# Kernel optimization log

Hardware: AMD Instinct MI355X
Metric: run time of the kernel (lower is better)

Reference implementation:

```python
import jax, jax.numpy as jnp
import numpy as np

N_NODES = 60000
N_EDGES = 120000
N_GRAPHS = 2048
ATOM_DIM = 4
H = 192            # hidden_dim
NL = 5             # n_layers
ND = 200           # n_descriptors
EDGE_DIM = 1


def setup_inputs() -> dict:
    key = jax.random.key(0)
    ks = jax.random.split(key, 16)

    def w(k, shape, fan_in):
        return jax.random.normal(k, shape, jnp.float32) * (1.0 / np.sqrt(fan_in))

    M_IN = 2 * H + EDGE_DIM  # message MLP input: [x_src, x_dst, edge_attr]
    M_H = 2 * H              # MPNNLayer(hidden_dim=hidden_dim*2)
    inp = {
        "atom_features": jax.random.normal(ks[0], (N_NODES, ATOM_DIM), jnp.float32),
        "edge_attr": jax.random.normal(ks[1], (N_EDGES, EDGE_DIM), jnp.float32),
        "edge_index": jax.random.randint(ks[2], (2, N_EDGES), 0, N_NODES),
        "batch": jnp.sort(jax.random.randint(ks[3], (N_NODES,), 0, N_GRAPHS)),
        # atom encoder: Linear + GELU + LayerNorm
        "enc_w": w(ks[4], (ATOM_DIM, H), ATOM_DIM), "enc_b": jnp.zeros((H,), jnp.float32),
        "enc_ln_g": jnp.ones((H,), jnp.float32), "enc_ln_b": jnp.zeros((H,), jnp.float32),
        # 5 MPNN layers (stacked params)
        "msg_w1": w(ks[5], (NL, M_IN, M_H), M_IN), "msg_b1": jnp.zeros((NL, M_H), jnp.float32),
        "msg_w2": w(ks[6], (NL, M_H, H), M_H), "msg_b2": jnp.zeros((NL, H), jnp.float32),
        "upd_w": w(ks[7], (NL, 2 * H, H), 2 * H), "upd_b": jnp.zeros((NL, H), jnp.float32),
        "ln_g": jnp.ones((NL, H), jnp.float32), "ln_b": jnp.zeros((NL, H), jnp.float32),
        # head MLP: 2H -> H -> H//2 -> ND
        "h1_w": w(ks[8], (2 * H, H), 2 * H), "h1_b": jnp.zeros((H,), jnp.float32),
        "h2_w": w(ks[9], (H, H // 2), H), "h2_b": jnp.zeros((H // 2,), jnp.float32),
        "h3_w": w(ks[10], (H // 2, ND), H // 2), "h3_b": jnp.zeros((ND,), jnp.float32),
    }
    return inp


def _ln(x, g, b, eps=1e-5):
    mu = x.mean(-1, keepdims=True)
    v = x.var(-1, keepdims=True)
    return (x - mu) / jnp.sqrt(v + eps) * g + b


def _gelu(x):
    return jax.nn.gelu(x, approximate=False)  # torch nn.GELU (erf)


def _forward(atom_features, edge_attr, enc_w, enc_b, enc_ln_g, enc_ln_b,
             msg_w1, msg_b1, msg_w2, msg_b2, upd_w, upd_b, ln_g, ln_b,
             h1_w, h1_b, h2_w, h2_b, h3_w, h3_b, edge_index, batch):
    src, dst = edge_index[0], edge_index[1]
    x = _ln(_gelu(atom_features @ enc_w + enc_b), enc_ln_g, enc_ln_b)  # [N, H]
    for l in range(NL):
        # gather endpoints -> message MLP -> scatter-sum to dst
        m_in = jnp.concatenate([x[src], x[dst], edge_attr], axis=-1)   # [E, 2H+1]
        m = _gelu(m_in @ msg_w1[l] + msg_b1[l]) @ msg_w2[l] + msg_b2[l]  # [E, H]
        agg = jax.ops.segment_sum(m, dst, num_segments=N_NODES)        # [N, H]
        x_new = _gelu(jnp.concatenate([x, agg], axis=-1) @ upd_w[l] + upd_b[l])
        x = _ln(x + x_new, ln_g[l], ln_b[l])  # residual + LN (dropout = eval identity)
    # per-graph mean/max pooling (segment reductions)
    cnt = jax.ops.segment_sum(jnp.ones((x.shape[0],), x.dtype), batch, num_segments=N_GRAPHS)
    s = jax.ops.segment_sum(x, batch, num_segments=N_GRAPHS)
    mean_pool = jnp.where(cnt[:, None] > 0, s / jnp.maximum(cnt, 1.0)[:, None], 0.0)
    max_pool = jax.ops.segment_max(x, batch, num_segments=N_GRAPHS)  # -inf for empty, as torch
    g = jnp.concatenate([mean_pool, max_pool], axis=-1)  # [G, 2H]
    h = _gelu(g @ h1_w + h1_b)
    h = _gelu(h @ h2_w + h2_b)
    return h @ h3_w + h3_b  # [G, ND]


def reference(atom_features, edge_attr, edge_index, batch, enc_w, enc_b, enc_ln_g, enc_ln_b,
              msg_w1, msg_b1, msg_w2, msg_b2, upd_w, upd_b, ln_g, ln_b,
              h1_w, h1_b, h2_w, h2_b, h3_w, h3_b):
    return _forward(atom_features, edge_attr, enc_w, enc_b, enc_ln_g, enc_ln_b,
                    msg_w1, msg_b1, msg_w2, msg_b2, upd_w, upd_b, ln_g, ln_b,
                    h1_w, h1_b, h2_w, h2_b, h3_w, h3_b, edge_index, batch)
```

## Files before the change

### kernel.cpp

```cpp
#include <hip/hip_runtime.h>

#define H 192
#define NL 5
#define NN 60000
#define NE 120000
#define NG 2048
#define ND 200
#define LDA 392
#define NT 128
#define LDU 200

typedef __bf16 bfrag __attribute__((ext_vector_type(8)));
typedef __bf16 bf16x4 __attribute__((ext_vector_type(4)));
typedef float f32x4 __attribute__((ext_vector_type(4)));

__device__ __forceinline__ unsigned short f2bf(float f) {
  union { float f; unsigned u; } v; v.f = f;
  return (unsigned short)((v.u + 0x7FFFu + ((v.u >> 16) & 1u)) >> 16);
}
__device__ __forceinline__ float bflo(unsigned u) {
  union { unsigned u; float f; } v; v.u = u << 16; return v.f;
}
__device__ __forceinline__ float bfhi(unsigned u) {
  union { unsigned u; float f; } v; v.u = u & 0xffff0000u; return v.f;
}
__device__ __forceinline__ float gelu(float x) {
  const float t = exp2f(x * (-2.3020922f - 0.10293942f * x * x));
  return x * __builtin_amdgcn_rcpf(1.f + t);
}

__global__ __launch_bounds__(256) void fold_kernel(
    const float* __restrict__ msg_w2, const float* __restrict__ upd_w,
    const float* __restrict__ msg_b2, float* __restrict__ W2p,
    float* __restrict__ v2) {
  __shared__ float row4[4][192];
  const int bid = blockIdx.x;
  const int l = bid / 97, sub = bid % 97;
  const int j = threadIdx.x;
  if (j < 192) {
    if (sub < 96) {
      const int k0 = sub * 4;
#pragma unroll
      for (int rr = 0; rr < 4; ++rr)
        row4[rr][j] = msg_w2[(size_t)l * 384 * 192 + (size_t)(k0 + rr) * 192 + j];
    } else {
      row4[0][j] = msg_b2[l * 192 + j];
    }
  }
  __syncthreads();
  if (j >= 192) return;
  const float* Ua = upd_w + (size_t)l * 384 * 192 + (size_t)192 * 192;
  float acc[4] = {0.f, 0.f, 0.f, 0.f};
  for (int t = 0; t < 192; ++t) {
    const float u = Ua[t * 192 + j];
#pragma unroll
    for (int rr = 0; rr < 4; ++rr) acc[rr] += row4[rr][t] * u;
  }
  if (sub < 96) {
    const int k0 = sub * 4;
#pragma unroll
    for (int rr = 0; rr < 4; ++rr)
      W2p[(size_t)l * 384 * 192 + (size_t)(k0 + rr) * 192 + j] = acc[rr];
  } else {
    v2[l * 192 + j] = acc[0];
  }
}

__global__ __launch_bounds__(256) void prep_kernel(
    const float* __restrict__ msg_w1, const float* __restrict__ W2p,
    const float* __restrict__ upd_w, const float* __restrict__ h1_w,
    const float* __restrict__ h2_w, const float* __restrict__ h3_w,
    unsigned short* __restrict__ W1f, float* __restrict__ w1last,
    unsigned short* __restrict__ W2f, unsigned short* __restrict__ Uxf,
    unsigned short* __restrict__ h1f, unsigned short* __restrict__ h2f,
    unsigned short* __restrict__ h3f) {
  int idx = blockIdx.x * 256 + threadIdx.x;
  const int SW1 = NL * 147456;
  const int S2 = NL * 384;
  const int SW2 = NL * 73728;
  const int SUX = NL * 36864;
  if (idx < SW1) {
    int l = idx / 147456, r = idx % 147456;
    int i = r & 7, lane = (r >> 3) & 63, t = r >> 9;
    int kk = t % 12, jblk = t / 12;
    int j = jblk * 16 + (lane & 15);
    int k = kk * 32 + ((lane >> 4) << 3) + i;
    W1f[idx] = f2bf(msg_w1[(size_t)l * 385 * 384 + (size_t)k * 384 + j]);
    return;
  }
  idx -= SW1;
  if (idx < S2) {
    int l = idx / 384, j = idx % 384;
    w1last[idx] = msg_w1[(size_t)l * 385 * 384 + 384 * 384 + j];
    return;
  }
  idx -= S2;
  if (idx < SW2) {
    int l = idx / 73728, r = idx % 73728;
    int i = r & 7, lane = (r >> 3) & 63, t = r >> 9;
    int kk = t % 12, jblk = t / 12;
    int j = jblk * 16 + (lane & 15);
    int k = kk * 32 + ((lane >> 4) << 3) + i;
    W2f[idx] = f2bf(W2p[(size_t)l * 384 * 192 + (size_t)k * 192 + j]);
    return;
  }
  idx -= SW2;
  if (idx < SUX) {
    int l = idx / 36864, r = idx % 36864;
    int i = r & 7, lane = (r >> 3) & 63, t = r >> 9;
    int kk = t % 6, jblk = t / 6;
    int j = jblk * 16 + (lane & 15);
    int k = kk * 32 + ((lane >> 4) << 3) + i;
    Uxf[idx] = f2bf(upd_w[(size_t)l * 384 * 192 + (size_t)k * 192 + j]);
    return;
  }
  idx -= SUX;
  if (idx < 73728) {
    int i = idx & 7, lane = (idx >> 3) & 63, t = idx >> 9;
    int kk = t % 12, jblk = t / 12;
    int j = jblk * 16 + (lane & 15);
    int k = kk * 32 + ((lane >> 4) << 3) + i;
    h1f[idx] = f2bf(h1_w[(size_t)k * 192 + j]);
    return;
  }
  idx -= 73728;
  if (idx < 18432) {
    int i = idx & 7, lane = (idx >> 3) & 63, t = idx >> 9;
    int kk = t % 6, jblk = t / 6;
    int j = jblk * 16 + (lane & 15);
    int k = kk * 32 + ((lane >> 4) << 3) + i;
    h2f[idx] = f2bf(h2_w[(size_t)k * 96 + j]);
    return;
  }
  idx -= 18432;
  if (idx < 19968) {
    int i = idx & 7, lane = (idx >> 3) & 63, t = idx >> 9;
    int kk = t % 3, jblk = t / 3;
    int j = jblk * 16 + (lane & 15);
    int k = kk * 32 + ((lane >> 4) << 3) + i;
    h3f[idx] = (j < 200) ? f2bf(h3_w[(size_t)k * 200 + j]) : (unsigned short)0;
    return;
  }
}

__global__ __launch_bounds__(256) void enc_kernel(
    const float* __restrict__ af, const float* __restrict__ w,
    const float* __restrict__ b, const float* __restrict__ g,
    const float* __restrict__ bb, __bf16* __restrict__ xb) {
  const int node = blockIdx.x * 4 + (threadIdx.x >> 6);
  const int lane = threadIdx.x & 63;
  if (node >= NN) return;
  const float a0 = af[node * 4 + 0], a1 = af[node * 4 + 1];
  const float a2 = af[node * 4 + 2], a3 = af[node * 4 + 3];
  float v[3], s = 0.f, ss = 0.f;
#pragma unroll
  for (int i = 0; i < 3; ++i) {
    const int j = lane + i * 64;
    float o = a0 * w[j] + a1 * w[H + j] + a2 * w[2 * H + j] + a3 * w[3 * H + j] + b[j];
    o = gelu(o);
    v[i] = o; s += o; ss += o * o;
  }
#pragma unroll
  for (int m = 1; m < 64; m <<= 1) { s += __shfl_xor(s, m); ss += __shfl_xor(ss, m); }
  const float mu = s * (1.f / H);
  float var = ss * (1.f / H) - mu * mu;
  const float rstd = rsqrtf(fmaxf(var, 0.f) + 1e-5f);
#pragma unroll
  for (int i = 0; i < 3; ++i) {
    const int j = lane + i * 64;
    xb[(size_t)node * H + j] = (__bf16)((v[i] - mu) * rstd * g[j] + bb[j]);
  }
}

__global__ __launch_bounds__(256) void csr_count(const int* __restrict__ ei,
                                                 int* __restrict__ deg) {
  const int e = blockIdx.x * 256 + threadIdx.x;
  if (e < NE) atomicAdd(&deg[ei[NE + e]], 1);
}

__global__ __launch_bounds__(1024) void csr_scan(const int* __restrict__ deg,
                                                 int* __restrict__ start) {
  __shared__ int wsum[16];
  const int tid = threadIdx.x, lane = tid & 63, wv = tid >> 6;
  int carry = 0;
  for (int base = 0; base < NN; base += 1024) {
    const int i = base + tid;
    int v = (i < NN) ? deg[i] : 0;
    int s = v;
#pragma unroll
    for (int d = 1; d < 64; d <<= 1) {
      int t = __shfl_up(s, d);
      if (lane >= d) s += t;
    }
    if (lane == 63) wsum[wv] = s;
    __syncthreads();
    if (wv == 0) {
      int ws_ = (lane < 16) ? wsum[lane] : 0;
#pragma unroll
      for (int d = 1; d < 16; d <<= 1) {
        int t = __shfl_up(ws_, d);
        if (lane >= d) ws_ += t;
      }
      if (lane < 16) wsum[lane] = ws_;
    }
    __syncthreads();
    const int woff = (wv == 0) ? 0 : wsum[wv - 1];
    if (i < NN) start[i] = carry + woff + s - v;
    carry += wsum[15];
    __syncthreads();
  }
  if (tid == 0) start[NN] = NE;
}

__global__ __launch_bounds__(256) void csr_fill(const int* __restrict__ ei,
                                                const int* __restrict__ start,
                                                int* __restrict__ cur,
                                                int* __restrict__ pos) {
  const int e = blockIdx.x * 256 + threadIdx.x;
  if (e < NE) {
    const int d = ei[NE + e];
    const int p = start[d] + atomicAdd(&cur[d], 1);
    pos[e] = p;
  }
}

__global__ __launch_bounds__(256) void gseg_kernel(const int* __restrict__ batch,
                                                   int* __restrict__ gstart,
                                                   int* __restrict__ gend) {
  const int i = blockIdx.x * 256 + threadIdx.x;
  if (i >= NN) return;
  const int b = batch[i];
  if (i == 0 || batch[i - 1] != b) gstart[b] = i;
  if (i == NN - 1 || batch[i + 1] != b) gend[b] = i + 1;
}

__global__ __launch_bounds__(512, 4) void msg_kernel(
    const __bf16* __restrict__ xb, const int* __restrict__ ei,
    const float* __restrict__ ea, const int* __restrict__ pos,
    const unsigned short* __restrict__ W1f, const float* __restrict__ w1last,
    const float* __restrict__ b1, const unsigned short* __restrict__ W2f,
    unsigned short* __restrict__ m) {
  __shared__ unsigned short A[64 * LDA];
  __shared__ float eaS[64];
  __shared__ int posS[64];
  const int tid = threadIdx.x;
  const int wave = tid >> 6, lane = tid & 63;
  const int lrow = lane & 15, kgrp = lane >> 4;
  const int tile = blockIdx.x * 64;

  if (tid < 64) {
    eaS[tid] = ea[tile + tid];
    posS[tid] = pos[tile + tid];
  }
  {
    const int r = tid >> 3, s = tid & 7;
    const int e = tile + r;
    const uint4* ps = (const uint4*)(xb + (size_t)ei[e] * H);
    const uint4* pd = (const uint4*)(xb + (size_t)ei[NE + e] * H);
#pragma unroll
    for (int i = 0; i < 3; ++i)
      *(uint4*)(&A[r * LDA + (s + 8 * i) * 8]) = ps[s + 8 * i];
#pragma unroll
    for (int i = 3; i < 6; ++i)
      *(uint4*)(&A[r * LDA + (s + 8 * i) * 8]) = pd[s + 8 * i - 24];
  }
  __syncthreads();

  const int jb16 = wave * 3;
  f32x4 acc[3][4];
#pragma unroll
  for (int mf = 0; mf < 3; ++mf)
#pragma unroll
    for (int eb = 0; eb < 4; ++eb)
#pragma unroll
      for (int q = 0; q < 4; ++q) acc[mf][eb][q] = 0.f;

#pragma unroll 2
  for (int kk = 0; kk < 12; ++kk) {
    const int k0 = kk * 32 + kgrp * 8;
    bfrag bF[4];
#pragma unroll
    for (int eb = 0; eb < 4; ++eb)
      bF[eb] = *(const bfrag*)(&A[(eb * 16 + lrow) * LDA + k0]);
#pragma unroll
    for (int mf = 0; mf < 3; ++mf) {
      const bfrag aF = *(const bfrag*)(W1f + ((size_t)((jb16 + mf) * 12 + kk) * 64 + lane) * 8);
#pragma unroll
      for (int eb = 0; eb < 4; ++eb)
        acc[mf][eb] = __builtin_amdgcn_mfma_f32_16x16x32_bf16(aF, bF[eb], acc[mf][eb], 0, 0, 0);
    }
  }
  __syncthreads();

#pragma unroll
  for (int mf = 0; mf < 3; ++mf) {
    const int j0 = (jb16 + mf) * 16 + kgrp * 4;
    const float bi0 = b1[j0], bi1 = b1[j0 + 1], bi2 = b1[j0 + 2], bi3 = b1[j0 + 3];
    const float wl0 = w1last[j0], wl1 = w1last[j0 + 1], wl2 = w1last[j0 + 2], wl3 = w1last[j0 + 3];
#pragma unroll
    for (int eb = 0; eb < 4; ++eb) {
      const int e = eb * 16 + lrow;
      const float eav = eaS[e];
      bf16x4 v;
      v[0] = (__bf16)gelu(acc[mf][eb][0] + bi0 + eav * wl0);
      v[1] = (__bf16)gelu(acc[mf][eb][1] + bi1 + eav * wl1);
      v[2] = (__bf16)gelu(acc[mf][eb][2] + bi2 + eav * wl2);
      v[3] = (__bf16)gelu(acc[mf][eb][3] + bi3 + eav * wl3);
      *(bf16x4*)(&A[e * LDA + j0]) = v;
    }
  }
  __syncthreads();

  const int jcnt2 = (wave < 4) ? 2 : 1;
  const int j2b0 = (wave < 4) ? (wave * 2) : (4 + wave);
  f32x4 acc2[2][4];
#pragma unroll
  for (int a = 0; a < 2; ++a)
#pragma unroll
    for (int eb = 0; eb < 4; ++eb)
#pragma unroll
      for (int q = 0; q < 4; ++q) acc2[a][eb][q] = 0.f;

#pragma unroll 2
  for (int kk = 0; kk < 12; ++kk) {
    const int k0 = kk * 32 + kgrp * 8;
    bfrag bF[4];
#pragma unroll
    for (int eb = 0; eb < 4; ++eb)
      bF[eb] = *(const bfrag*)(&A[(eb * 16 + lrow) * LDA + k0]);
#pragma unroll
    for (int a = 0; a < 2; ++a) {
      if (a < jcnt2) {
        const bfrag aF = *(const bfrag*)(W2f + ((size_t)((j2b0 + a) * 12 + kk) * 64 + lane) * 8);
#pragma unroll
        for (int eb = 0; eb < 4; ++eb)
          acc2[a][eb] = __builtin_amdgcn_mfma_f32_16x16x32_bf16(aF, bF[eb], acc2[a][eb], 0, 0, 0);
      }
    }
  }
#pragma unroll
  for (int a = 0; a < 2; ++a) {
    if (a < jcnt2) {
      const int j0 = (j2b0 + a) * 16 + kgrp * 4;
#pragma unroll
      for (int eb = 0; eb < 4; ++eb) {
        const int e = eb * 16 + lrow;
        bf16x4 v;
        v[0] = (__bf16)acc2[a][eb][0];
        v[1] = (__bf16)acc2[a][eb][1];
        v[2] = (__bf16)acc2[a][eb][2];
        v[3] = (__bf16)acc2[a][eb][3];
        *(bf16x4*)(m + (size_t)posS[e] * H + j0) = v;
      }
    }
  }
}

__global__ __launch_bounds__(512, 4) void upd_kernel(
    const unsigned short* __restrict__ Uxf, const float* __restrict__ ub,
    const float* __restrict__ v2, const float* __restrict__ lng,
    const float* __restrict__ lnb, const unsigned short* __restrict__ m,
    const int* __restrict__ start, __bf16* xb) {
  __shared__ unsigned short A[NT * LDU];
  __shared__ float wsm[8][NT];
  __shared__ float wsq[8][NT];
  __shared__ float mur[NT], rsr[NT];
  __shared__ float degS[NT];
  const int tid = threadIdx.x;
  const int wave = tid >> 6, lane = tid & 63;
  const int lrow = lane & 15, kgrp = lane >> 4;
  const int tile = blockIdx.x * NT;

  const int r = tid >> 2, q4 = tid & 3;
  const int node = tile + r;
  if (node < NN) {
    const uint4* px = (const uint4*)(xb + (size_t)node * H + q4 * 48);
#pragma unroll
    for (int i = 0; i < 6; ++i)
      *(uint4*)(&A[r * LDU + q4 * 48 + i * 8]) = px[i];
  } else {
#pragma unroll
    for (int i = 0; i < 6; ++i)
      *(uint4*)(&A[r * LDU + q4 * 48 + i * 8]) = make_uint4(0, 0, 0, 0);
  }
  __syncthreads();

  const int jcnt = (wave < 4) ? 2 : 1;
  const int jb0 = (wave < 4) ? (wave * 2) : (4 + wave);

  f32x4 acc[2][8];
#pragma unroll
  for (int a = 0; a < 2; ++a)
#pragma unroll
    for (int eb = 0; eb < 8; ++eb)
#pragma unroll
      for (int q = 0; q < 4; ++q) acc[a][eb][q] = 0.f;

#pragma unroll 1
  for (int kk = 0; kk < 6; ++kk) {
    const int k0 = kk * 32 + kgrp * 8;
    bfrag bF[8];
#pragma unroll
    for (int eb = 0; eb < 8; ++eb)
      bF[eb] = *(const bfrag*)(&A[(eb * 16 + lrow) * LDU + k0]);
#pragma unroll
    for (int a = 0; a < 2; ++a) {
      if (a < jcnt) {
        const bfrag aF = *(const bfrag*)(Uxf + ((size_t)((jb0 + a) * 6 + kk) * 64 + lane) * 8);
#pragma unroll
        for (int eb = 0; eb < 8; ++eb)
          acc[a][eb] = __builtin_amdgcn_mfma_f32_16x16x32_bf16(aF, bF[eb], acc[a][eb], 0, 0, 0);
      }
    }
  }
  __syncthreads();

  if (node < NN) {
    const int p0 = start[node], p1 = start[node + 1];
    if (q4 == 0) degS[r] = (float)(p1 - p0);
#pragma unroll
    for (int hh = 0; hh < 2; ++hh) {
      const int c0 = q4 * 48 + hh * 24;
      float av[24];
#pragma unroll
      for (int i = 0; i < 24; ++i) av[i] = 0.f;
      for (int p = p0; p < p1; ++p) {
        const uint4* mr = (const uint4*)(m + (size_t)p * H + c0);
#pragma unroll
        for (int i = 0; i < 3; ++i) {
          const uint4 u = mr[i];
          av[i * 8 + 0] += bflo(u.x); av[i * 8 + 1] += bfhi(u.x);
          av[i * 8 + 2] += bflo(u.y); av[i * 8 + 3] += bfhi(u.y);
          av[i * 8 + 4] += bflo(u.z); av[i * 8 + 5] += bfhi(u.z);
          av[i * 8 + 6] += bflo(u.w); av[i * 8 + 7] += bfhi(u.w);
        }
      }
#pragma unroll
      for (int i = 0; i < 24; i += 4) {
        bf16x4 v;
        v[0] = (__bf16)av[i]; v[1] = (__bf16)av[i + 1];
        v[2] = (__bf16)av[i + 2]; v[3] = (__bf16)av[i + 3];
        *(bf16x4*)(&A[r * LDU + c0 + i]) = v;
      }
    }
  } else {
    if (q4 == 0) degS[r] = 0.f;
#pragma unroll
    for (int i = 0; i < 48; i += 8)
      *(uint4*)(&A[r * LDU + q4 * 48 + i]) = make_uint4(0, 0, 0, 0);
  }
  __syncthreads();

  float lsum[8], lsq[8];
#pragma unroll
  for (int eb = 0; eb < 8; ++eb) { lsum[eb] = 0.f; lsq[eb] = 0.f; }
#pragma unroll
  for (int a = 0; a < 2; ++a) {
    if (a < jcnt) {
      const int jb = (jb0 + a) * 16 + kgrp * 4;
      const float4 ub4 = *(const float4*)(ub + jb);
      const float4 v24 = *(const float4*)(v2 + jb);
#pragma unroll
      for (int eb = 0; eb < 8; ++eb) {
        const int nc = eb * 16 + lrow;
        const int n2 = tile + nc;
        if (n2 < NN) {
          const bf16x4 ag = *(const bf16x4*)(&A[nc * LDU + jb]);
          const float d = degS[nc];
          const bf16x4 xr = *(const bf16x4*)(xb + (size_t)n2 * H + jb);
          acc[a][eb][0] = (float)xr[0] + gelu(acc[a][eb][0] + (float)ag[0] + d * v24.x + ub4.x);
          acc[a][eb][1] = (float)xr[1] + gelu(acc[a][eb][1] + (float)ag[1] + d * v24.y + ub4.y);
          acc[a][eb][2] = (float)xr[2] + gelu(acc[a][eb][2] + (float)ag[2] + d * v24.z + ub4.z);
          acc[a][eb][3] = (float)xr[3] + gelu(acc[a][eb][3] + (float)ag[3] + d * v24.w + ub4.w);
        } else {
          acc[a][eb][0] = 0.f; acc[a][eb][1] = 0.f;
          acc[a][eb][2] = 0.f; acc[a][eb][3] = 0.f;
        }
#pragma unroll
        for (int q = 0; q < 4; ++q) {
          lsum[eb] += acc[a][eb][q];
          lsq[eb] += acc[a][eb][q] * acc[a][eb][q];
        }
      }
    }
  }
#pragma unroll
  for (int eb = 0; eb < 8; ++eb) {
    lsum[eb] += __shfl_xor(lsum[eb], 16);
    lsum[eb] += __shfl_xor(lsum[eb], 32);
    lsq[eb] += __shfl_xor(lsq[eb], 16);
    lsq[eb] += __shfl_xor(lsq[eb], 32);
  }
  if (kgrp == 0) {
#pragma unroll
    for (int eb = 0; eb < 8; ++eb) {
      wsm[wave][eb * 16 + lrow] = lsum[eb];
      wsq[wave][eb * 16 + lrow] = lsq[eb];
    }
  }
  __syncthreads();
  if (tid < NT) {
    float s = 0.f, sq = 0.f;
#pragma unroll
    for (int w2 = 0; w2 < 8; ++w2) { s += wsm[w2][tid]; sq += wsq[w2][tid]; }
    const float mu = s * (1.f / H);
    float var = sq * (1.f / H) - mu * mu;
    mur[tid] = mu;
    rsr[tid] = rsqrtf(fmaxf(var, 0.f) + 1e-5f);
  }
  __syncthreads();
#pragma unroll
  for (int a = 0; a < 2; ++a) {
    if (a < jcnt) {
      const int jb = (jb0 + a) * 16 + kgrp * 4;
      const float4 g4 = *(const float4*)(lng + jb);
      const float4 b4 = *(const float4*)(lnb + jb);
#pragma unroll
      for (int eb = 0; eb < 8; ++eb) {
        const int nc = eb * 16 + lrow;
        const int n2 = tile + nc;
        if (n2 < NN) {
          const float mu = mur[nc], rs = rsr[nc];
          bf16x4 ob;
          ob[0] = (__bf16)((acc[a][eb][0] - mu) * rs * g4.x + b4.x);
          ob[1] = (__bf16)((acc[a][eb][1] - mu) * rs * g4.y + b4.y);
          ob[2] = (__bf16)((acc[a][eb][2] - mu) * rs * g4.z + b4.z);
          ob[3] = (__bf16)((acc[a][eb][3] - mu) * rs * g4.w + b4.w);
          *(bf16x4*)(xb + (size_t)n2 * H + jb) = ob;
        }
      }
    }
  }
}

__global__ __launch_bounds__(256) void pool_kernel(
    const __bf16* __restrict__ xb, const int* __restrict__ gstart,
    const int* __restrict__ gend, __bf16* __restrict__ Gb) {
  const int w = threadIdx.x >> 6, lane = threadIdx.x & 63;
  const int gi = blockIdx.x * 4 + w;
  const int n0 = gstart[gi], n1 = gend[gi];
  float sm[3] = {0.f, 0.f, 0.f};
  float mx[3] = {-INFINITY, -INFINITY, -INFINITY};
  for (int n = n0; n < n1; ++n) {
#pragma unroll
    for (int i = 0; i < 3; ++i) {
      const float v = (float)xb[(size_t)n * H + lane + i * 64];
      sm[i] += v; mx[i] = fmaxf(mx[i], v);
    }
  }
  const int cnt = n1 - n0;
  const float inv = cnt > 0 ? 1.f / (float)cnt : 0.f;
#pragma unroll
  for (int i = 0; i < 3; ++i) {
    const int j = lane + i * 64;
    Gb[(size_t)gi * 384 + j] = (__bf16)(sm[i] * inv);
    Gb[(size_t)gi * 384 + 192 + j] = (__bf16)mx[i];
  }
}

__global__ __launch_bounds__(512) void head_kernel(
    const __bf16* __restrict__ Gb,
    const unsigned short* __restrict__ h1f, const float* __restrict__ h1b,
    const unsigned short* __restrict__ h2f, const float* __restrict__ h2b,
    const unsigned short* __restrict__ h3f, const float* __restrict__ h3b,
    float* __restrict__ out) {
  __shared__ unsigned short A[32 * LDA];
  const int tid = threadIdx.x;
  const int wave = tid >> 6, lane = tid & 63;
  const int lrow = lane & 15, kgrp = lane >> 4;
  const int tile = blockIdx.x * 32;

  {
    const int r = tid >> 4, s = tid & 15;
    const uint4* pg = (const uint4*)(Gb + (size_t)(tile + r) * 384);
#pragma unroll
    for (int i = 0; i < 3; ++i)
      *(uint4*)(&A[r * LDA + (s + 16 * i) * 8]) = pg[s + 16 * i];
  }
  __syncthreads();

  const int jcnt1 = (wave < 4) ? 2 : 1;
  const int jb1 = (wave < 4) ? (wave * 2) : (4 + wave);
  f32x4 acc[2][2];
#pragma unroll
  for (int a = 0; a < 2; ++a)
#pragma unroll
    for (int eb = 0; eb < 2; ++eb)
#pragma unroll
      for (int q = 0; q < 4; ++q) acc[a][eb][q] = 0.f;
#pragma unroll 2
  for (int kk = 0; kk < 12; ++kk) {
    const int k0 = kk * 32 + kgrp * 8;
    bfrag bF[2];
#pragma unroll
    for (int eb = 0; eb < 2; ++eb)
      bF[eb] = *(const bfrag*)(&A[(eb * 16 + lrow) * LDA + k0]);
#pragma unroll
    for (int a = 0; a < 2; ++a) {
      if (a < jcnt1) {
        const bfrag aF = *(const bfrag*)(h1f + ((size_t)((jb1 + a) * 12 + kk) * 64 + lane) * 8);
#pragma unroll
        for (int eb = 0; eb < 2; ++eb)
          acc[a][eb] = __builtin_amdgcn_mfma_f32_16x16x32_bf16(aF, bF[eb], acc[a][eb], 0, 0, 0);
      }
    }
  }
  __syncthreads();
#pragma unroll
  for (int a = 0; a < 2; ++a) {
    if (a < jcnt1) {
      const int j0 = (jb1 + a) * 16 + kgrp * 4;
      const float4 b4 = *(const float4*)(h1b + j0);
#pragma unroll
      for (int eb = 0; eb < 2; ++eb) {
        const int g = eb * 16 + lrow;
        bf16x4 v;
        v[0] = (__bf16)gelu(acc[a][eb][0] + b4.x);
        v[1] = (__bf16)gelu(acc[a][eb][1] + b4.y);
        v[2] = (__bf16)gelu(acc[a][eb][2] + b4.z);
        v[3] = (__bf16)gelu(acc[a][eb][3] + b4.w);
        *(bf16x4*)(&A[g * LDA + j0]) = v;
      }
    }
  }
  __syncthreads();

  f32x4 acc2[2];
#pragma unroll
  for (int eb = 0; eb < 2; ++eb)
#pragma unroll
    for (int q = 0; q < 4; ++q) acc2[eb][q] = 0.f;
  if (wave < 6) {
#pragma unroll 2
    for (int kk = 0; kk < 6; ++kk) {
      const int k0 = kk * 32 + kgrp * 8;
      bfrag bF[2];
#pragma unroll
      for (int eb = 0; eb < 2; ++eb)
        bF[eb] = *(const bfrag*)(&A[(eb * 16 + lrow) * LDA + k0]);
      const bfrag aF = *(const bfrag*)(h2f + ((size_t)(wave * 6 + kk) * 64 + lane) * 8);
#pragma unroll
      for (int eb = 0; eb < 2; ++eb)
        acc2[eb] = __builtin_amdgcn_mfma_f32_16x16x32_bf16(aF, bF[eb], acc2[eb], 0, 0, 0);
    }
  }
  __syncthreads();
  if (wave < 6) {
    const int j0 = wave * 16 + kgrp * 4;
    const float4 b4 = *(const float4*)(h2b + j0);
#pragma unroll
    for (int eb = 0; eb < 2; ++eb) {
      const int g = eb * 16 + lrow;
      bf16x4 v;
      v[0] = (__bf16)gelu(acc2[eb][0] + b4.x);
      v[1] = (__bf16)gelu(acc2[eb][1] + b4.y);
      v[2] = (__bf16)gelu(acc2[eb][2] + b4.z);
      v[3] = (__bf16)gelu(acc2[eb][3] + b4.w);
      *(bf16x4*)(&A[g * LDA + 192 + j0]) = v;
    }
  }
  __syncthreads();

  const int jcnt3 = (wave < 5) ? 2 : 1;
  const int jb3 = (wave < 5) ? (wave * 2) : (wave + 5);
  f32x4 acc3[2][2];
#pragma unroll
  for (int a = 0; a < 2; ++a)
#pragma unroll
    for (int eb = 0; eb < 2; ++eb)
#pragma unroll
      for (int q = 0; q < 4; ++q) acc3[a][eb][q] = 0.f;
#pragma unroll
  for (int kk = 0; kk < 3; ++kk) {
    const int k0 = 192 + kk * 32 + kgrp * 8;
    bfrag bF[2];
#pragma unroll
    for (int eb = 0; eb < 2; ++eb)
      bF[eb] = *(const bfrag*)(&A[(eb * 16 + lrow) * LDA + k0]);
#pragma unroll
    for (int a = 0; a < 2; ++a) {
      if (a < jcnt3) {
        const bfrag aF = *(const bfrag*)(h3f + ((size_t)((jb3 + a) * 3 + kk) * 64 + lane) * 8);
#pragma unroll
        for (int eb = 0; eb < 2; ++eb)
          acc3[a][eb] = __builtin_amdgcn_mfma_f32_16x16x32_bf16(aF, bF[eb], acc3[a][eb], 0, 0, 0);
      }
    }
  }
#pragma unroll
  for (int a = 0; a < 2; ++a) {
    if (a < jcnt3) {
      const int jb = jb3 + a;
      const int j0 = jb * 16 + kgrp * 4;
#pragma unroll
      for (int eb = 0; eb < 2; ++eb) {
        const int g = tile + eb * 16 + lrow;
        if (jb < 12) {
          const float4 b4 = *(const float4*)(h3b + j0);
          float4 o;
          o.x = acc3[a][eb][0] + b4.x;
          o.y = acc3[a][eb][1] + b4.y;
          o.z = acc3[a][eb][2] + b4.z;
          o.w = acc3[a][eb][3] + b4.w;
          *(float4*)(out + (size_t)g * ND + j0) = o;
        } else {
#pragma unroll
          for (int t = 0; t < 4; ++t) {
            const int j = j0 + t;
            if (j < ND) out[(size_t)g * ND + j] = acc3[a][eb][t] + h3b[j];
          }
        }
      }
    }
  }
}

extern "C" void kernel_launch(void* const* d_in, const int* in_sizes, int n_in,
                              void* d_out, int out_size, void* d_ws, size_t ws_size,
                              hipStream_t stream) {
  const float* atom   = (const float*)d_in[0];
  const float* ea     = (const float*)d_in[1];
  const int*   ei     = (const int*)d_in[2];
  const int*   batch  = (const int*)d_in[3];
  const float* enc_w  = (const float*)d_in[4];
  const float* enc_b  = (const float*)d_in[5];
  const float* enc_lng= (const float*)d_in[6];
  const float* enc_lnb= (const float*)d_in[7];
  const float* msg_w1 = (const float*)d_in[8];
  const float* msg_b1 = (const float*)d_in[9];
  const float* msg_w2 = (const float*)d_in[10];
  const float* msg_b2 = (const float*)d_in[11];
  const float* upd_w  = (const float*)d_in[12];
  const float* upd_b  = (const float*)d_in[13];
  const float* ln_g   = (const float*)d_in[14];
  const float* ln_b   = (const float*)d_in[15];
  const float* h1_w   = (const float*)d_in[16];
  const float* h1_b   = (const float*)d_in[17];
  const float* h2_w   = (const float*)d_in[18];
  const float* h2_b   = (const float*)d_in[19];
  const float* h3_w   = (const float*)d_in[20];
  const float* h3_b   = (const float*)d_in[21];
  float* out = (float*)d_out;

  char* ws = (char*)d_ws;
  size_t off = 0;
  auto alloc = [&](size_t bytes) -> void* {
    void* p = ws + off;
    off = (off + bytes + 255) & ~(size_t)255;
    return p;
  };
  __bf16* xb          = (__bf16*)alloc((size_t)NN * H * 2);
  unsigned short* msg = (unsigned short*)alloc((size_t)NE * H * 2);
  unsigned short* W1f = (unsigned short*)alloc((size_t)NL * 147456 * 2);
  float* w1last       = (float*)alloc((size_t)NL * 384 * 4);
  unsigned short* W2f = (unsigned short*)alloc((size_t)NL * 73728 * 2);
  unsigned short* Uxf = (unsigned short*)alloc((size_t)NL * 36864 * 2);
  float* W2p          = (float*)alloc((size_t)NL * 384 * 192 * 4);
  float* v2           = (float*)alloc((size_t)NL * 192 * 4);
  unsigned short* h1f = (unsigned short*)alloc((size_t)73728 * 2);
  unsigned short* h2f = (unsigned short*)alloc((size_t)18432 * 2);
  unsigned short* h3f = (unsigned short*)alloc((size_t)19968 * 2);
  __bf16* Gb          = (__bf16*)alloc((size_t)NG * 384 * 2);
  int* deg            = (int*)alloc((size_t)NN * 4);
  int* cstart         = (int*)alloc((size_t)(NN + 1) * 4);
  int* pos            = (int*)alloc((size_t)NE * 4);
  int* gstart         = (int*)alloc((size_t)NG * 4);
  int* gend           = (int*)alloc((size_t)NG * 4);

  fold_kernel<<<NL * 97, 256, 0, stream>>>(msg_w2, upd_w, msg_b2, W2p, v2);
  prep_kernel<<<5486, 256, 0, stream>>>(msg_w1, W2p, upd_w, h1_w, h2_w, h3_w,
                                        W1f, w1last, W2f, Uxf, h1f, h2f, h3f);
  enc_kernel<<<NN / 4, 256, 0, stream>>>(atom, enc_w, enc_b, enc_lng, enc_lnb, xb);

  hipMemsetAsync(deg, 0, (size_t)NN * 4, stream);
  csr_count<<<(NE + 255) / 256, 256, 0, stream>>>(ei, deg);
  csr_scan<<<1, 1024, 0, stream>>>(deg, cstart);
  hipMemsetAsync(deg, 0, (size_t)NN * 4, stream);
  csr_fill<<<(NE + 255) / 256, 256, 0, stream>>>(ei, cstart, deg, pos);

  hipMemsetAsync(gstart, 0, (size_t)NG * 4, stream);
  hipMemsetAsync(gend, 0, (size_t)NG * 4, stream);
  gseg_kernel<<<(NN + 255) / 256, 256, 0, stream>>>(batch, gstart, gend);

  for (int l = 0; l < NL; ++l) {
    msg_kernel<<<NE / 64, 512, 0, stream>>>(
        xb, ei, ea, pos, W1f + (size_t)l * 147456, w1last + l * 384,
        msg_b1 + l * 384, W2f + (size_t)l * 73728, msg);
    upd_kernel<<<(NN + NT - 1) / NT, 512, 0, stream>>>(
        Uxf + (size_t)l * 36864, upd_b + l * 192, v2 + l * 192,
        ln_g + l * 192, ln_b + l * 192, msg, cstart, xb);
  }
  pool_kernel<<<NG / 4, 256, 0, stream>>>(xb, gstart, gend, Gb);
  head_kernel<<<NG / 32, 512, 0, stream>>>(Gb, h1f, h1_b, h2f, h2_b, h3f, h3_b, out);
}
```

Before: 756.5 us.

## Make msg_kernel persistent and prefetch next tile's gathered rows into registers

The message kernel now launches a fixed grid of 512 blocks that loop over 64-edge tiles, instead of one block per tile. While the MLP for the current tile runs, each thread loads the next tile's source and destination node rows, edge attributes and positions into registers, then writes them to shared memory once the tile is finished. The goal is to hide the latency of the random gathers behind the MFMA work. In exchange it raises register pressure with six uint4 values per thread, and 512 blocks may leave some CUs underused at launch_bounds(512,4).

```diff
diff --git a/kernel.cpp b/kernel.cpp
--- a/kernel.cpp
+++ b/kernel.cpp
@@ -9,6 +9,7 @@
 #define LDA 392
 #define NT 128
 #define LDU 200
+#define MSGB 512
 
 typedef __bf16 bfrag __attribute__((ext_vector_type(8)));
 typedef __bf16 bf16x4 __attribute__((ext_vector_type(4)));
@@ -246,112 +247,139 @@
   const int tid = threadIdx.x;
   const int wave = tid >> 6, lane = tid & 63;
   const int lrow = lane & 15, kgrp = lane >> 4;
-  const int tile = blockIdx.x * 64;
-
-  if (tid < 64) {
-    eaS[tid] = ea[tile + tid];
-    posS[tid] = pos[tile + tid];
-  }
+  const int sr = tid >> 3, sc = tid & 7;
+  const int NTILES = NE / 64;
+
   {
-    const int r = tid >> 3, s = tid & 7;
-    const int e = tile + r;
+    const int tile = blockIdx.x * 64;
+    if (tid < 64) { eaS[tid] = ea[tile + tid]; posS[tid] = pos[tile + tid]; }
+    const int e = tile + sr;
     const uint4* ps = (const uint4*)(xb + (size_t)ei[e] * H);
     const uint4* pd = (const uint4*)(xb + (size_t)ei[NE + e] * H);
 #pragma unroll
     for (int i = 0; i < 3; ++i)
-      *(uint4*)(&A[r * LDA + (s + 8 * i) * 8]) = ps[s + 8 * i];
+      *(uint4*)(&A[sr * LDA + (sc + 8 * i) * 8]) = ps[sc + 8 * i];
 #pragma unroll
     for (int i = 3; i < 6; ++i)
-      *(uint4*)(&A[r * LDA + (s + 8 * i) * 8]) = pd[s + 8 * i - 24];
-  }
-  __syncthreads();
-
-  const int jb16 = wave * 3;
-  f32x4 acc[3][4];
-#pragma unroll
-  for (int mf = 0; mf < 3; ++mf)
-#pragma unroll
-    for (int eb = 0; eb < 4; ++eb)
-#pragma unroll
-      for (int q = 0; q < 4; ++q) acc[mf][eb][q] = 0.f;
+      *(uint4*)(&A[sr * LDA + (sc + 8 * i) * 8]) = pd[sc + 8 * i - 24];
+  }
+  __syncthreads();
+
+  for (int tile_idx = blockIdx.x; tile_idx < NTILES; tile_idx += MSGB) {
+    const int tile = tile_idx * 64;
+    const bool has_next = (tile_idx + MSGB) < NTILES;
+
+    uint4 pf[6];
+    float eaN = 0.f;
+    int posN = 0;
+    if (has_next) {
+      const int t2 = (tile_idx + MSGB) * 64;
+      const int e2 = t2 + sr;
+      const uint4* ps = (const uint4*)(xb + (size_t)ei[e2] * H);
+      const uint4* pd = (const uint4*)(xb + (size_t)ei[NE + e2] * H);
+#pragma unroll
+      for (int i = 0; i < 3; ++i) pf[i] = ps[sc + 8 * i];
+#pragma unroll
+      for (int i = 3; i < 6; ++i) pf[i] = pd[sc + 8 * i - 24];
+      if (tid < 64) { eaN = ea[t2 + tid]; posN = pos[t2 + tid]; }
+    }
+
+    const int jb16 = wave * 3;
+    f32x4 acc[3][4];
+#pragma unroll
+    for (int mf = 0; mf < 3; ++mf)
+#pragma unroll
+      for (int eb = 0; eb < 4; ++eb)
+#pragma unroll
+        for (int q = 0; q < 4; ++q) acc[mf][eb][q] = 0.f;
 
 #pragma unroll 2
-  for (int kk = 0; kk < 12; ++kk) {
-    const int k0 = kk * 32 + kgrp * 8;
-    bfrag bF[4];
-#pragma unroll
-    for (int eb = 0; eb < 4; ++eb)
-      bF[eb] = *(const bfrag*)(&A[(eb * 16 + lrow) * LDA + k0]);
+    for (int kk = 0; kk < 12; ++kk) {
+      const int k0 = kk * 32 + kgrp * 8;
+      bfrag bF[4];
+#pragma unroll
+      for (int eb = 0; eb < 4; ++eb)
+        bF[eb] = *(const bfrag*)(&A[(eb * 16 + lrow) * LDA + k0]);
+#pragma unroll
+      for (int mf = 0; mf < 3; ++mf) {
+        const bfrag aF = *(const bfrag*)(W1f + ((size_t)((jb16 + mf) * 12 + kk) * 64 + lane) * 8);
+#pragma unroll
+        for (int eb = 0; eb < 4; ++eb)
+          acc[mf][eb] = __builtin_amdgcn_mfma_f32_16x16x32_bf16(aF, bF[eb], acc[mf][eb], 0, 0, 0);
+      }
+    }
+    __syncthreads();
+
 #pragma unroll
     for (int mf = 0; mf < 3; ++mf) {
-      const bfrag aF = *(const bfrag*)(W1f + ((size_t)((jb16 + mf) * 12 + kk) * 64 + lane) * 8);
+      const int j0 = (jb16 + mf) * 16 + kgrp * 4;
+      const float bi0 = b1[j0], bi1 = b1[j0 + 1], bi2 = b1[j0 + 2], bi3 = b1[j0 + 3];
+      const float wl0 = w1last[j0], wl1 = w1last[j0 + 1], wl2 = w1last[j0 + 2], wl3 = w1last[j0 + 3];
+#pragma unroll
+      for (int eb = 0; eb < 4; ++eb) {
+        const int e = eb * 16 + lrow;
+        const float eav = eaS[e];
+        bf16x4 v;
+        v[0] = (__bf16)gelu(acc[mf][eb][0] + bi0 + eav * wl0);
+        v[1] = (__bf16)gelu(acc[mf][eb][1] + bi1 + eav * wl1);
+        v[2] = (__bf16)gelu(acc[mf][eb][2] + bi2 + eav * wl2);
+        v[3] = (__bf16)gelu(acc[mf][eb][3] + bi3 + eav * wl3);
+        *(bf16x4*)(&A[e * LDA + j0]) = v;
+      }
+    }
+    __syncthreads();
+
+    const int jcnt2 = (wave < 4) ? 2 : 1;
+    const int j2b0 = (wave < 4) ? (wave * 2) : (4 + wave);
+    f32x4 acc2[2][4];
+#pragma unroll
+    for (int a = 0; a < 2; ++a)
 #pragma unroll
       for (int eb = 0; eb < 4; ++eb)
-        acc[mf][eb] = __builtin_amdgcn_mfma_f32_16x16x32_bf16(aF, bF[eb], acc[mf][eb], 0, 0, 0);
-    }
-  }
-  __syncthreads();
-
-#pragma unroll
-  for (int mf = 0; mf < 3; ++mf) {
-    const int j0 = (jb16 + mf) * 16 + kgrp * 4;
-    const float bi0 = b1[j0], bi1 = b1[j0 + 1], bi2 = b1[j0 + 2], bi3 = b1[j0 + 3];
-    const float wl0 = w1last[j0], wl1 = w1last[j0 + 1], wl2 = w1last[j0 + 2], wl3 = w1last[j0 + 3];
-#pragma unroll
-    for (int eb = 0; eb < 4; ++eb) {
-      const int e = eb * 16 + lrow;
-      const float eav = eaS[e];
-      bf16x4 v;
-      v[0] = (__bf16)gelu(acc[mf][eb][0] + bi0 + eav * wl0);
-      v[1] = (__bf16)gelu(acc[mf][eb][1] + bi1 + eav * wl1);
-      v[2] = (__bf16)gelu(acc[mf][eb][2] + bi2 + eav * wl2);
-      v[3] = (__bf16)gelu(acc[mf][eb][3] + bi3 + eav * wl3);
-      *(bf16x4*)(&A[e * LDA + j0]) = v;
-    }
-  }
-  __syncthreads();
-
-  const int jcnt2 = (wave < 4) ? 2 : 1;
-  const int j2b0 = (wave < 4) ? (wave * 2) : (4 + wave);
-  f32x4 acc2[2][4];
-#pragma unroll
-  for (int a = 0; a < 2; ++a)
-#pragma unroll
-    for (int eb = 0; eb < 4; ++eb)
-#pragma unroll
-      for (int q = 0; q < 4; ++q) acc2[a][eb][q] = 0.f;
+#pragma unroll
+        for (int q = 0; q < 4; ++q) acc2[a][eb][q] = 0.f;
 
 #pragma unroll 2
-  for (int kk = 0; kk < 12; ++kk) {
-    const int k0 = kk * 32 + kgrp * 8;
-    bfrag bF[4];
-#pragma unroll
-    for (int eb = 0; eb < 4; ++eb)
-      bF[eb] = *(const bfrag*)(&A[(eb * 16 + lrow) * LDA + k0]);
+    for (int kk = 0; kk < 12; ++kk) {
+      const int k0 = kk * 32 + kgrp * 8;
+      bfrag bF[4];
+#pragma unroll
+      for (int eb = 0; eb < 4; ++eb)
+        bF[eb] = *(const bfrag*)(&A[(eb * 16 + lrow) * LDA + k0]);
+#pragma unroll
+      for (int a = 0; a < 2; ++a) {
+        if (a < jcnt2) {
+          const bfrag aF = *(const bfrag*)(W2f + ((size_t)((j2b0 + a) * 12 + kk) * 64 + lane) * 8);
+#pragma unroll
+          for (int eb = 0; eb < 4; ++eb)
+            acc2[a][eb] = __builtin_amdgcn_mfma_f32_16x16x32_bf16(aF, bF[eb], acc2[a][eb], 0, 0, 0);
+        }
+      }
+    }
 #pragma unroll
     for (int a = 0; a < 2; ++a) {
       if (a < jcnt2) {
-        const bfrag aF = *(const bfrag*)(W2f + ((size_t)((j2b0 + a) * 12 + kk) * 64 + lane) * 8);
-#pragma unroll
-        for (int eb = 0; eb < 4; ++eb)
-          acc2[a][eb] = __builtin_amdgcn_mfma_f32_16x16x32_bf16(aF, bF[eb], acc2[a][eb], 0, 0, 0);
-      }
-    }
-  }
-#pragma unroll
-  for (int a = 0; a < 2; ++a) {
-    if (a < jcnt2) {
-      const int j0 = (j2b0 + a) * 16 + kgrp * 4;
-#pragma unroll
-      for (int eb = 0; eb < 4; ++eb) {
-        const int e = eb * 16 + lrow;
-        bf16x4 v;
-        v[0] = (__bf16)acc2[a][eb][0];
-        v[1] = (__bf16)acc2[a][eb][1];
-        v[2] = (__bf16)acc2[a][eb][2];
-        v[3] = (__bf16)acc2[a][eb][3];
-        *(bf16x4*)(m + (size_t)posS[e] * H + j0) = v;
-      }
+        const int j0 = (j2b0 + a) * 16 + kgrp * 4;
+#pragma unroll
+        for (int eb = 0; eb < 4; ++eb) {
+          const int e = eb * 16 + lrow;
+          bf16x4 v;
+          v[0] = (__bf16)acc2[a][eb][0];
+          v[1] = (__bf16)acc2[a][eb][1];
+          v[2] = (__bf16)acc2[a][eb][2];
+          v[3] = (__bf16)acc2[a][eb][3];
+          *(bf16x4*)(m + (size_t)posS[e] * H + j0) = v;
+        }
+      }
+    }
+    __syncthreads();
+
+    if (has_next) {
+#pragma unroll
+      for (int i = 0; i < 6; ++i)
+        *(uint4*)(&A[sr * LDA + (sc + 8 * i) * 8]) = pf[i];
+      if (tid < 64) { eaS[tid] = eaN; posS[tid] = posN; }
+      __syncthreads();
     }
   }
 }
@@ -783,7 +811,7 @@
   gseg_kernel<<<(NN + 255) / 256, 256, 0, stream>>>(batch, gstart, gend);
 
   for (int l = 0; l < NL; ++l) {
-    msg_kernel<<<NE / 64, 512, 0, stream>>>(
+    msg_kernel<<<MSGB, 512, 0, stream>>>(
         xb, ei, ea, pos, W1f + (size_t)l * 147456, w1last + l * 384,
         msg_b1 + l * 384, W2f + (size_t)l * 73728, msg);
     upd_kernel<<<(NN + NT - 1) / NT, 512, 0, stream>>>(
```

Measured after the change: 894.3 us. 18.2% more time.
